# Optimization experiments

Hardware: AMD Instinct MI355X
Metric: run time of the kernel (lower is better)

The kernel has to match this reference:

```python
import jax, jax.numpy as jnp
import numpy as np

NTOKENS = 50257
NHID = 1024
TPC = int(np.ceil(np.sqrt(NTOKENS)))          # 225 tokens per class
NCLASSES = int(np.ceil(NTOKENS / TPC))        # 224 classes
BATCH = 2048
INITRANGE = 0.1


def setup_inputs() -> dict:
    key = jax.random.key(0)
    k1, k2, k3, k4 = jax.random.split(key, 4)
    inputs = jax.random.normal(k1, (BATCH, NHID), dtype=jnp.float32)
    labels = jax.random.randint(k2, (BATCH,), 0, NTOKENS, dtype=jnp.int32)
    W_top = jax.random.uniform(k3, (NHID, NCLASSES), dtype=jnp.float32,
                               minval=-INITRANGE, maxval=INITRANGE)
    b_top = jnp.zeros((NCLASSES,), dtype=jnp.float32)
    W_bottom = jax.random.uniform(k4, (NCLASSES, NHID, TPC), dtype=jnp.float32,
                                  minval=-INITRANGE, maxval=INITRANGE)
    b_bottom = jnp.zeros((NCLASSES, TPC), dtype=jnp.float32)
    return {"inputs": inputs, "labels": labels, "W_top": W_top, "b_top": b_top,
            "W_bottom": W_bottom, "b_bottom": b_bottom}


def reference(inputs, labels, W_top, b_top, W_bottom, b_bottom):
    # Two-level hierarchical softmax: P(word) = P(class | h) * P(word | class, h)
    batch = inputs.shape[0]
    cls = labels // TPC          # [B] class index at top level
    word = labels % TPC          # [B] word index within class

    # Top level: [B, nclasses]
    top_probs = jax.nn.softmax(inputs @ W_top + b_top, axis=1)
    p_cls = top_probs[jnp.arange(batch), cls]            # [B]

    # Bottom level: gather per-example class weights then batched matvec
    Wb = W_bottom[cls]                                    # [B, nhid, tpc]
    bb = b_bottom[cls]                                    # [B, tpc]
    bottom_logits = jnp.einsum('bd,bdk->bk', inputs, Wb) + bb
    bottom_probs = jax.nn.softmax(bottom_logits, axis=1)
    p_word = bottom_probs[jnp.arange(batch), word]        # [B]

    return p_cls * p_word
```

## Files before the change

kernel.cpp:

```cpp
#include <hip/hip_runtime.h>
#include <math.h>

#define TPC 225
#define NCLS 224
#define NHID 1024
#define BATCH 2048
#define CAP 256
#define LSTRIDE 256
#define NCHUNK 8
#define CHUNK_D 128
#define NDQ 32

__global__ __launch_bounds__(256) void hs_bucket(const int* __restrict__ labels,
                                                 int* __restrict__ bucket,
                                                 int* __restrict__ cnt) {
    __shared__ int scnt[NCLS];
    const int t = threadIdx.x;
    for (int i = t; i < NCLS; i += 256) scnt[i] = 0;
    __syncthreads();
    for (int b = t; b < BATCH; b += 256) {
        int lab = labels[b];
        int c = lab / TPC;
        int pos = atomicAdd(&scnt[c], 1);
        bucket[c * CAP + pos] = b;
    }
    __syncthreads();
    for (int i = t; i < NCLS; i += 256) cnt[i] = scnt[i];
}

#define LOADW(W)                                              \
    do {                                                      \
        _Pragma("unroll") for (int di = 0; di < 4; di++)      \
            _Pragma("unroll") for (int j = 0; j < 4; j++)     \
                W[di][j] = pj[j][di * KS];                    \
        _Pragma("unroll") for (int j = 0; j < 4; j++)         \
            pj[j] += 4 * KS;                                  \
    } while (0)

#define LOADX(X, dq)                                          \
    do {                                                      \
        _Pragma("unroll") for (int rl = 0; rl < RW; rl++)     \
            X[rl] = *(const float4*)(xp[rl] + (dq) * 4);      \
    } while (0)

#define FMAS(W, X)                                            \
    do {                                                      \
        _Pragma("unroll") for (int rl = 0; rl < RW; rl++) {   \
            _Pragma("unroll") for (int di = 0; di < 4; di++) {\
                float xv = ((const float*)&X[rl])[di];        \
                _Pragma("unroll") for (int j = 0; j < 4; j++) \
                    acc[rl][j] = fmaf(xv, W[di][j], acc[rl][j]); \
            }                                                 \
        }                                                     \
    } while (0)

template <int RW, int KS>
__device__ __forceinline__ void gemm_chunk(const float* __restrict__ xb,
                                           const int* rows,
                                           const float* __restrict__ wq,
                                           const int lane,
                                           float acc[RW][4]) {
    const float* xp[RW];
#pragma unroll
    for (int rl = 0; rl < RW; rl++) xp[rl] = xb + (size_t)rows[rl] * NHID;
    const float* pj[4];
#pragma unroll
    for (int j = 0; j < 4; j++) {
        int k = 64 * j + lane;
        pj[j] = wq + (k < KS ? k : KS - 1);
    }
#pragma unroll
    for (int rl = 0; rl < RW; rl++)
#pragma unroll
        for (int j = 0; j < 4; j++) acc[rl][j] = 0.f;

    float wA[4][4], wB[4][4];
    float4 xA[RW], xB[RW];
    LOADW(wA);
    LOADX(xA, 0);
    for (int dq = 0; dq < NDQ; dq += 2) {
        LOADW(wB);
        LOADX(xB, dq + 1);
        FMAS(wA, xA);
        if (dq + 2 < NDQ) {
            LOADW(wA);
            LOADX(xA, dq + 2);
        }
        FMAS(wB, xB);
    }
}

__global__ __launch_bounds__(256, 4) void hs_tlogits(const float* __restrict__ x,
                                                     const float* __restrict__ W,
                                                     float* __restrict__ twsP) {
    const int rb = blockIdx.x >> 3;
    const int q = blockIdx.x & 7;
    const int lane = threadIdx.x & 63;
    const int wr = threadIdx.x >> 6;
    int rows[4];
#pragma unroll
    for (int rl = 0; rl < 4; rl++) rows[rl] = rb * 16 + wr * 4 + rl;
    const float* xb = x + q * CHUNK_D;
    const float* wq = W + (size_t)q * CHUNK_D * NCLS;
    float acc[4][4];
    gemm_chunk<4, NCLS>(xb, rows, wq, lane, acc);
    float* tp = twsP + (size_t)q * BATCH * LSTRIDE;
#pragma unroll
    for (int rl = 0; rl < 4; rl++)
#pragma unroll
        for (int j = 0; j < 4; j++) {
            int k = 64 * j + lane;
            if (k < NCLS) tp[(size_t)rows[rl] * LSTRIDE + k] = acc[rl][j];
        }
}

template <int RW>
__device__ __forceinline__ void bchunk(const float* __restrict__ xb,
                                       const float* __restrict__ wq,
                                       const int* __restrict__ bucket_c,
                                       const int base, const int n,
                                       const int lane, const int wr,
                                       float* __restrict__ bp) {
    int rows[RW], rval[RW];
#pragma unroll
    for (int rl = 0; rl < RW; rl++) {
        int idx = base + wr * RW + rl;
        rows[rl] = bucket_c[idx < n ? idx : 0];
        rval[rl] = (idx < n);
    }
    float acc[RW][4];
    gemm_chunk<RW, TPC>(xb, rows, wq, lane, acc);
#pragma unroll
    for (int rl = 0; rl < RW; rl++) {
        if (rval[rl]) {
#pragma unroll
            for (int j = 0; j < 4; j++) {
                int k = 64 * j + lane;
                if (k < TPC) bp[(size_t)rows[rl] * LSTRIDE + k] = acc[rl][j];
            }
        }
    }
}

__global__ __launch_bounds__(256, 4) void hs_blogits(const float* __restrict__ x,
                                                     const float* __restrict__ Wb,
                                                     const int* __restrict__ bucket,
                                                     const int* __restrict__ cnt,
                                                     float* __restrict__ bws) {
    const int c = blockIdx.x >> 3;
    const int q = blockIdx.x & 7;
    const int n = cnt[c];
    if (n == 0) return;
    const int lane = threadIdx.x & 63;
    const int wr = threadIdx.x >> 6;
    const float* wq = Wb + (size_t)c * (NHID * TPC) + (size_t)q * CHUNK_D * TPC;
    const float* xb = x + q * CHUNK_D;
    const int* bucket_c = bucket + c * CAP;
    float* bp = bws + (size_t)q * BATCH * LSTRIDE;

    for (int base = 0; base < n; base += 16) {
        int m = n - base;
        if (m > 16) m = 16;
        const int RW = (m + 3) >> 2;
        switch (RW) {
            case 1: bchunk<1>(xb, wq, bucket_c, base, n, lane, wr, bp); break;
            case 2: bchunk<2>(xb, wq, bucket_c, base, n, lane, wr, bp); break;
            case 3: bchunk<3>(xb, wq, bucket_c, base, n, lane, wr, bp); break;
            default: bchunk<4>(xb, wq, bucket_c, base, n, lane, wr, bp); break;
        }
    }
}

__global__ __launch_bounds__(256) void hs_finish(const float* __restrict__ tws,
                                                 const float* __restrict__ bws,
                                                 const int* __restrict__ labels,
                                                 const float* __restrict__ b_top,
                                                 const float* __restrict__ b_bot,
                                                 float* __restrict__ out) {
    const int lane = threadIdx.x & 63;
    const int wave = threadIdx.x >> 6;
    const int row = blockIdx.x * 4 + wave;
    const int label = labels[row];
    const int c = label / TPC;
    const int word = label - c * TPC;

    float p[2];
#pragma unroll
    for (int lvl = 0; lvl < 2; lvl++) {
        const int NS = lvl ? TPC : NCLS;
        const int pick = lvl ? word : c;
        const float* lws = lvl ? bws : tws;
        const float* bias = lvl ? (b_bot + c * TPC) : b_top;
        float lg[4];
#pragma unroll
        for (int j = 0; j < 4; j++) {
            int k = lane + 64 * j;
            if (k < NS) {
                float v = 0.f;
#pragma unroll
                for (int pq = 0; pq < NCHUNK; pq++)
                    v += lws[((size_t)pq * BATCH + row) * LSTRIDE + k];
                lg[j] = v + bias[k];
            } else {
                lg[j] = -INFINITY;
            }
        }
        float m = fmaxf(fmaxf(lg[0], lg[1]), fmaxf(lg[2], lg[3]));
#pragma unroll
        for (int off = 32; off > 0; off >>= 1) m = fmaxf(m, __shfl_xor(m, off, 64));
        float s = 0.f, pp = 0.f;
#pragma unroll
        for (int j = 0; j < 4; j++) {
            int k = lane + 64 * j;
            float e = (k < NS) ? __expf(lg[j] - m) : 0.f;
            s += e;
            if (k == pick) pp = e;
        }
#pragma unroll
        for (int off = 32; off > 0; off >>= 1) {
            s += __shfl_xor(s, off, 64);
            pp += __shfl_xor(pp, off, 64);
        }
        p[lvl] = pp / s;
    }
    if (lane == 0) out[row] = p[0] * p[1];
}

extern "C" void kernel_launch(void* const* d_in, const int* in_sizes, int n_in,
                              void* d_out, int out_size, void* d_ws, size_t ws_size,
                              hipStream_t stream) {
    const float* inputs   = (const float*)d_in[0];
    const int*   labels   = (const int*)d_in[1];
    const float* W_top    = (const float*)d_in[2];
    const float* b_top    = (const float*)d_in[3];
    const float* W_bottom = (const float*)d_in[4];
    const float* b_bottom = (const float*)d_in[5];
    float* out = (float*)d_out;

    int* bucket = (int*)d_ws;
    int* cnt    = bucket + NCLS * CAP;
    float* tws  = (float*)(cnt + NCLS);
    float* bws  = tws + (size_t)NCHUNK * BATCH * LSTRIDE;

    hs_bucket<<<1, 256, 0, stream>>>(labels, bucket, cnt);
    hs_tlogits<<<128 * NCHUNK, 256, 0, stream>>>(inputs, W_top, tws);
    hs_blogits<<<NCLS * NCHUNK, 256, 0, stream>>>(inputs, W_bottom, bucket, cnt, bws);
    hs_finish<<<BATCH / 4, 256, 0, stream>>>(tws, bws, labels, b_top, b_bottom, out);
}
```

Measured before the change: 431.0 us.

## Stage top weights in LDS and vectorize bottom-level weight loads

The top-level logits kernel now loads a 64-row slice of W_top into shared memory per block, covering 32 batch rows with 512 threads, and splits the hidden dimension into 16 chunks instead of 8. The bottom-level kernel switches from strided scalar weight loads to float4 loads with four contiguous columns per lane, plus a float4 store, and drops the software double-buffering. The aim is fewer redundant global weight reads and more efficient memory transactions. In exchange, the finish kernel must sum 16 partial slices for the top level, which doubles the top workspace traffic.

```diff
diff --git a/kernel.cpp b/kernel.cpp
--- a/kernel.cpp
+++ b/kernel.cpp
@@ -7,9 +7,15 @@
 #define BATCH 2048
 #define CAP 256
 #define LSTRIDE 256
+
 #define NCHUNK 8
 #define CHUNK_D 128
 #define NDQ 32
+
+#define TCH 16
+#define TCH_D 64
+#define TROWS 32
+#define TPAD 228
 
 __global__ __launch_bounds__(256) void hs_bucket(const int* __restrict__ labels,
                                                  int* __restrict__ bucket,
@@ -28,88 +34,67 @@
     for (int i = t; i < NCLS; i += 256) cnt[i] = scnt[i];
 }
 
-#define LOADW(W)                                              \
-    do {                                                      \
-        _Pragma("unroll") for (int di = 0; di < 4; di++)      \
-            _Pragma("unroll") for (int j = 0; j < 4; j++)     \
-                W[di][j] = pj[j][di * KS];                    \
-        _Pragma("unroll") for (int j = 0; j < 4; j++)         \
-            pj[j] += 4 * KS;                                  \
-    } while (0)
-
-#define LOADX(X, dq)                                          \
-    do {                                                      \
-        _Pragma("unroll") for (int rl = 0; rl < RW; rl++)     \
-            X[rl] = *(const float4*)(xp[rl] + (dq) * 4);      \
-    } while (0)
-
-#define FMAS(W, X)                                            \
-    do {                                                      \
-        _Pragma("unroll") for (int rl = 0; rl < RW; rl++) {   \
-            _Pragma("unroll") for (int di = 0; di < 4; di++) {\
-                float xv = ((const float*)&X[rl])[di];        \
-                _Pragma("unroll") for (int j = 0; j < 4; j++) \
-                    acc[rl][j] = fmaf(xv, W[di][j], acc[rl][j]); \
-            }                                                 \
-        }                                                     \
-    } while (0)
-
-template <int RW, int KS>
-__device__ __forceinline__ void gemm_chunk(const float* __restrict__ xb,
-                                           const int* rows,
-                                           const float* __restrict__ wq,
-                                           const int lane,
-                                           float acc[RW][4]) {
-    const float* xp[RW];
-#pragma unroll
-    for (int rl = 0; rl < RW; rl++) xp[rl] = xb + (size_t)rows[rl] * NHID;
-    const float* pj[4];
-#pragma unroll
-    for (int j = 0; j < 4; j++) {
-        int k = 64 * j + lane;
-        pj[j] = wq + (k < KS ? k : KS - 1);
-    }
-#pragma unroll
-    for (int rl = 0; rl < RW; rl++)
-#pragma unroll
-        for (int j = 0; j < 4; j++) acc[rl][j] = 0.f;
-
-    float wA[4][4], wB[4][4];
-    float4 xA[RW], xB[RW];
-    LOADW(wA);
-    LOADX(xA, 0);
-    for (int dq = 0; dq < NDQ; dq += 2) {
-        LOADW(wB);
-        LOADX(xB, dq + 1);
-        FMAS(wA, xA);
-        if (dq + 2 < NDQ) {
-            LOADW(wA);
-            LOADX(xA, dq + 2);
-        }
-        FMAS(wB, xB);
-    }
-}
-
-__global__ __launch_bounds__(256, 4) void hs_tlogits(const float* __restrict__ x,
+__global__ __launch_bounds__(512, 2) void hs_tlogits(const float* __restrict__ x,
                                                      const float* __restrict__ W,
                                                      float* __restrict__ twsP) {
-    const int rb = blockIdx.x >> 3;
-    const int q = blockIdx.x & 7;
-    const int lane = threadIdx.x & 63;
-    const int wr = threadIdx.x >> 6;
+    __shared__ float lw[TCH_D * TPAD];
+    const int rb = blockIdx.x >> 4;
+    const int q = blockIdx.x & 15;
+    const int t = threadIdx.x;
+    const int lane = t & 63;
+    const int wv = t >> 6;
+
+    for (int r = wv; r < TCH_D; r += 8) {
+        if (lane < 56) {
+            float4 v = *(const float4*)(W + (size_t)(q * TCH_D + r) * NCLS + 4 * lane);
+            *(float4*)(&lw[r * TPAD + 4 * lane]) = v;
+        }
+    }
+    __syncthreads();
+
     int rows[4];
 #pragma unroll
-    for (int rl = 0; rl < 4; rl++) rows[rl] = rb * 16 + wr * 4 + rl;
-    const float* xb = x + q * CHUNK_D;
-    const float* wq = W + (size_t)q * CHUNK_D * NCLS;
-    float acc[4][4];
-    gemm_chunk<4, NCLS>(xb, rows, wq, lane, acc);
+    for (int rl = 0; rl < 4; rl++) rows[rl] = rb * TROWS + wv * 4 + rl;
+    const float* xp[4];
+#pragma unroll
+    for (int rl = 0; rl < 4; rl++)
+        xp[rl] = x + (size_t)rows[rl] * NHID + q * TCH_D;
+    int kcl[4];
+#pragma unroll
+    for (int j = 0; j < 4; j++) {
+        int k = lane + 64 * j;
+        kcl[j] = (k < NCLS) ? k : (NCLS - 1);
+    }
+
+    float acc[4][4] = {};
+    for (int dq = 0; dq < TCH_D / 4; ++dq) {
+        float w[4][4];
+#pragma unroll
+        for (int di = 0; di < 4; di++)
+#pragma unroll
+            for (int j = 0; j < 4; j++)
+                w[di][j] = lw[(dq * 4 + di) * TPAD + kcl[j]];
+        float4 xq[4];
+#pragma unroll
+        for (int rl = 0; rl < 4; rl++)
+            xq[rl] = *(const float4*)(xp[rl] + dq * 4);
+#pragma unroll
+        for (int rl = 0; rl < 4; rl++)
+#pragma unroll
+            for (int di = 0; di < 4; di++) {
+                float xv = ((const float*)&xq[rl])[di];
+#pragma unroll
+                for (int j = 0; j < 4; j++)
+                    acc[rl][j] = fmaf(xv, w[di][j], acc[rl][j]);
+            }
+    }
+
     float* tp = twsP + (size_t)q * BATCH * LSTRIDE;
 #pragma unroll
     for (int rl = 0; rl < 4; rl++)
 #pragma unroll
         for (int j = 0; j < 4; j++) {
-            int k = 64 * j + lane;
+            int k = lane + 64 * j;
             if (k < NCLS) tp[(size_t)rows[rl] * LSTRIDE + k] = acc[rl][j];
         }
 }
@@ -128,16 +113,39 @@
         rows[rl] = bucket_c[idx < n ? idx : 0];
         rval[rl] = (idx < n);
     }
-    float acc[RW][4];
-    gemm_chunk<RW, TPC>(xb, rows, wq, lane, acc);
+    const float* xp[RW];
+#pragma unroll
+    for (int rl = 0; rl < RW; rl++) xp[rl] = xb + (size_t)rows[rl] * NHID;
+    const int kb = (4 * lane <= TPC - 4) ? 4 * lane : (TPC - 4);
+    const float* pw = wq + kb;
+
+    float acc[RW][4] = {};
+    for (int dq = 0; dq < NDQ; ++dq) {
+        float4 wv4[4];
+#pragma unroll
+        for (int di = 0; di < 4; di++)
+            wv4[di] = *(const float4*)(pw + di * TPC);
+        pw += 4 * TPC;
+        float4 xq[RW];
+#pragma unroll
+        for (int rl = 0; rl < RW; rl++)
+            xq[rl] = *(const float4*)(xp[rl] + dq * 4);
+#pragma unroll
+        for (int rl = 0; rl < RW; rl++)
+#pragma unroll
+            for (int di = 0; di < 4; di++) {
+                const float xv = ((const float*)&xq[rl])[di];
+                acc[rl][0] = fmaf(xv, wv4[di].x, acc[rl][0]);
+                acc[rl][1] = fmaf(xv, wv4[di].y, acc[rl][1]);
+                acc[rl][2] = fmaf(xv, wv4[di].z, acc[rl][2]);
+                acc[rl][3] = fmaf(xv, wv4[di].w, acc[rl][3]);
+            }
+    }
 #pragma unroll
     for (int rl = 0; rl < RW; rl++) {
         if (rval[rl]) {
-#pragma unroll
-            for (int j = 0; j < 4; j++) {
-                int k = 64 * j + lane;
-                if (k < TPC) bp[(size_t)rows[rl] * LSTRIDE + k] = acc[rl][j];
-            }
+            *(float4*)(bp + (size_t)rows[rl] * LSTRIDE + kb) =
+                make_float4(acc[rl][0], acc[rl][1], acc[rl][2], acc[rl][3]);
         }
     }
 }
@@ -188,6 +196,7 @@
 #pragma unroll
     for (int lvl = 0; lvl < 2; lvl++) {
         const int NS = lvl ? TPC : NCLS;
+        const int NP = lvl ? NCHUNK : TCH;
         const int pick = lvl ? word : c;
         const float* lws = lvl ? bws : tws;
         const float* bias = lvl ? (b_bot + c * TPC) : b_top;
@@ -197,8 +206,7 @@
             int k = lane + 64 * j;
             if (k < NS) {
                 float v = 0.f;
-#pragma unroll
-                for (int pq = 0; pq < NCHUNK; pq++)
+                for (int pq = 0; pq < NP; pq++)
                     v += lws[((size_t)pq * BATCH + row) * LSTRIDE + k];
                 lg[j] = v + bias[k];
             } else {
@@ -240,10 +248,10 @@
     int* bucket = (int*)d_ws;
     int* cnt    = bucket + NCLS * CAP;
     float* tws  = (float*)(cnt + NCLS);
-    float* bws  = tws + (size_t)NCHUNK * BATCH * LSTRIDE;
+    float* bws  = tws + (size_t)TCH * BATCH * LSTRIDE;
 
     hs_bucket<<<1, 256, 0, stream>>>(labels, bucket, cnt);
-    hs_tlogits<<<128 * NCHUNK, 256, 0, stream>>>(inputs, W_top, tws);
+    hs_tlogits<<<64 * TCH, 512, 0, stream>>>(inputs, W_top, tws);
     hs_blogits<<<NCLS * NCHUNK, 256, 0, stream>>>(inputs, W_bottom, bucket, cnt, bws);
     hs_finish<<<BATCH / 4, 256, 0, stream>>>(tws, bws, labels, b_top, b_bottom, out);
 }
```

Measured after the change: 494.7 us. +14.8%, slower.
